# Optimization experiments

Measured on AMD Instinct MI355X. Metric: run time of the kernel, lower is better.

Reference implementation:

```python
import jax, jax.numpy as jnp
import numpy as np

K = 3
KK = K * K
PAD = 1          # kernel_size // 2
MAX_SHIFT = 8.0  # bias_range > 0
DEG = 2          # degrees = (2, 2), paon_type 'a'


def setup_inputs() -> dict:
    key = jax.random.key(0)
    ks = jax.random.split(key, 6)
    B, C, O, H, W = 4, 64, 64, 160, 160
    x = jax.random.normal(ks[0], (B, C, H, W), jnp.float32)
    # offset conv is 1x1: weight [2*K*K, C], bias [2*K*K]
    off_w = jax.random.normal(ks[1], (2 * KK, C), jnp.float32) * 0.1
    off_b = jax.random.normal(ks[2], (2 * KK,), jnp.float32) * 0.1
    scale = 1.0 / np.sqrt(C * KK).astype(np.float32)
    w_m = jax.random.normal(ks[3], (DEG * O, C, K, K), jnp.float32) * scale
    w_n = jax.random.normal(ks[4], (DEG * O, C, K, K), jnp.float32) * scale
    w0 = jax.random.normal(ks[5], (O,), jnp.float32) * 0.1
    return {"x": x, "off_w": off_w, "off_b": off_b, "w_m": w_m, "w_n": w_n, "w0": w0}


def _bilinear_sample(x, py, px):
    """x: [B,C,H,W]; py,px: [B,KK,H,W] -> [B,C,KK,H,W]; zero outside bounds."""
    B, C, H, W = x.shape
    xf = x.reshape(B, C, H * W)
    y0 = jnp.floor(py)
    x0 = jnp.floor(px)
    wy = py - y0
    wx = px - x0
    y0i = y0.astype(jnp.int32)
    x0i = x0.astype(jnp.int32)
    out = jnp.zeros((B, C) + py.shape[1:], x.dtype)
    corners = ((0, 0, (1 - wy) * (1 - wx)), (0, 1, (1 - wy) * wx),
               (1, 0, wy * (1 - wx)), (1, 1, wy * wx))
    for dy, dx, wgt in corners:
        yy = y0i + dy
        xx = x0i + dx
        valid = (yy >= 0) & (yy < H) & (xx >= 0) & (xx < W)
        idx = jnp.clip(yy, 0, H - 1) * W + jnp.clip(xx, 0, W - 1)
        g = jax.vmap(lambda f, i: f[:, i])(xf, idx.reshape(B, -1))  # [B,C,KK*H*W]
        out = out + g.reshape(B, C, *py.shape[1:]) * (wgt * valid)[:, None]
    return out


def _after_poly_a(y, ch, o, take_abs):
    # channel reorder + groupwise sum, per PaLaBase.after_poly_a
    order = np.array([(k * ch) % (ch * o) + k // o for k in range(ch * o)])
    y = y[:, order].reshape(y.shape[0], ch, o, *y.shape[2:])
    return jnp.abs(y).sum(2) if take_abs else y.sum(2)


def reference(x, off_w, off_b, w_m, w_n, w0):
    B, C, H, W = x.shape
    O = w0.shape[0]
    # --- DeformOffset: 1x1 conv -> clamp to image -> tanh soft-limit ---
    off_r = jnp.einsum('bchw,oc->bohw', x, off_w) + off_b[None, :, None, None]
    gy = jnp.arange(H, dtype=x.dtype)[None, None, :, None]
    gx = jnp.arange(W, dtype=x.dtype)[None, None, None, :]
    oy = jnp.clip(off_r[:, 0::2], -gy, H - gy)  # [B,KK,H,W] (dy per kernel pos)
    ox = jnp.clip(off_r[:, 1::2], -gx, W - gx)  # [B,KK,H,W] (dx per kernel pos)
    soft = lambda o: jnp.where(jnp.abs(o) >= MAX_SHIFT,
                               MAX_SHIFT * jnp.tanh(o / MAX_SHIFT), o)
    oy, ox = soft(oy), soft(ox)
    # --- deformable sampling grid (stride=1, dilation=1, zero padding) ---
    kidx = jnp.arange(KK)
    kh = (kidx // K).astype(x.dtype)[None, :, None, None]
    kw = (kidx % K).astype(x.dtype)[None, :, None, None]
    base_y = (jnp.arange(H, dtype=x.dtype) - PAD)[None, None, :, None]
    base_x = (jnp.arange(W, dtype=x.dtype) - PAD)[None, None, None, :]
    py = base_y + kh + oy
    px = base_x + kw + ox
    samp = _bilinear_sample(x, py, px)  # [B,C,KK,H,W]
    # --- Pade numerator / denominator convs on the sampled tensor ---
    pm_raw = jnp.einsum('bckhw,ock->bohw', samp, w_m.reshape(DEG * O, C, KK))
    qn_raw = jnp.einsum('bckhw,ock->bohw', samp, w_n.reshape(DEG * O, C, KK))
    pm = _after_poly_a(pm_raw, O, DEG, take_abs=False)
    qn = _after_poly_a(qn_raw, O, DEG, take_abs=True)
    # prepare_for_div_a: (pm + w0, 1 + qn)
    return (pm + w0[None, :, None, None]) / (1.0 + qn)
```

## Files before the change

kernel.cpp:

```cpp
#include <hip/hip_runtime.h>
#include <hip/hip_bf16.h>
#include <hip/hip_fp16.h>

#define Hh 160
#define Ww 160
#define Cc 64
#define HWc 25600
#define Bb 4
#define AST 76

typedef __attribute__((ext_vector_type(8))) _Float16 half8;
typedef __attribute__((ext_vector_type(4))) float f32x4;

__device__ __forceinline__ unsigned int f2h2u(float a, float b) {
  __half2 h = __floats2half2_rn(a, b);
  return *(unsigned int*)&h;
}

__global__ __launch_bounds__(256) void k_prep(
    const float* __restrict__ x, const float* __restrict__ wm,
    const float* __restrict__ wn, const float* __restrict__ ow,
    unsigned short* __restrict__ xT, unsigned short* __restrict__ bf) {
  if (blockIdx.x < 400) {
    __shared__ unsigned short s[64][260];
    int wg = blockIdx.x;
    int b = wg / 100;
    int pix0 = (wg % 100) * 256;
    int l = threadIdx.x & 63, wv = threadIdx.x >> 6;
    const float* xb = x + (size_t)b * Cc * HWc + pix0;
#pragma unroll
    for (int i = 0; i < 16; i++) {
      int c = i * 4 + wv;
      float4 v = *(const float4*)&xb[(size_t)c * HWc + l * 4];
      *(uint2*)&s[c][l * 4] = make_uint2(f2h2u(v.x, v.y), f2h2u(v.z, v.w));
    }
    __syncthreads();
    int p = threadIdx.x;
    unsigned int w[32];
#pragma unroll
    for (int j = 0; j < 32; j++) {
      unsigned int a = s[2 * j][p];
      unsigned int bb = s[2 * j + 1][p];
      w[j] = (a & 0xffffu) | (bb << 16);
    }
    unsigned short* dst = xT + ((size_t)(b * HWc + pix0 + p)) * 64;
#pragma unroll
    for (int j = 0; j < 8; j++)
      ((uint4*)dst)[j] = make_uint4(w[4 * j], w[4 * j + 1], w[4 * j + 2], w[4 * j + 3]);
  } else {
    int i = (blockIdx.x - 400) * 256 + threadIdx.x;
    if (i < 9 * 2 * 12 * 64 * 8) {
      int j2 = i & 7;
      int lane = (i >> 3) & 63;
      int ntck = i >> 9;
      int nt = ntck % 12;
      int ck = ntck / 12;
      int kk = ck >> 1;
      int chunk = ck & 1;
      int n = nt * 16 + (lane & 15);
      int c = chunk * 32 + (lane >> 4) * 8 + j2;
      float v;
      if (n < 64)
        v = wm[(n * 64 + c) * 9 + kk] + wm[((n + 64) * 64 + c) * 9 + kk];
      else
        v = wn[((n - 64) * 64 + c) * 9 + kk];
      __half hv = __float2half_rn(v);
      bf[i] = *(unsigned short*)&hv;
    } else if (i < 9 * 2 * 12 * 64 * 8 + 2 * 2 * 64 * 8) {
      int j = i - 9 * 2 * 12 * 64 * 8;
      int j2 = j & 7;
      int lane = (j >> 3) & 63;
      int rest = j >> 9;
      int ntile = rest & 1;
      int chunk = rest >> 1;
      int n = ntile * 16 + (lane & 15);
      int c = chunk * 32 + (lane >> 4) * 8 + j2;
      if (n < 18) {
        __half hv = __float2half_rn(ow[n * 64 + c]);
        bf[i] = *(unsigned short*)&hv;
      } else {
        bf[i] = 0;
      }
    }
  }
}

__device__ __forceinline__ void gather2h(const char* __restrict__ gbase, uint4 D,
                                         int chB, uint4& c00, uint4& c01,
                                         uint4& c10, uint4& c11, __half2& W00,
                                         __half2& W01, __half2& W10,
                                         __half2& W11) {
  int bb = (int)D.x + chB;
  int dxB = (int)(D.y & 0xffffu);
  int dyB = (int)(D.y >> 16);
  c00 = *(const uint4*)(gbase + bb);
  c01 = *(const uint4*)(gbase + bb + dxB);
  c10 = *(const uint4*)(gbase + bb + dyB);
  c11 = *(const uint4*)(gbase + bb + dxB + dyB);
  __half2 wz = *(const __half2*)&D.z;
  __half2 ww = *(const __half2*)&D.w;
  W00 = __half2half2(__low2half(wz));
  W01 = __half2half2(__high2half(wz));
  W10 = __half2half2(__low2half(ww));
  W11 = __half2half2(__high2half(ww));
}

__device__ __forceinline__ void combine_write(unsigned short* Arow,
                                              const uint4& c00, const uint4& c01,
                                              const uint4& c10, const uint4& c11,
                                              __half2 W00, __half2 W01,
                                              __half2 W10, __half2 W11) {
  const unsigned int* a = (const unsigned int*)&c00;
  const unsigned int* b = (const unsigned int*)&c01;
  const unsigned int* c = (const unsigned int*)&c10;
  const unsigned int* d = (const unsigned int*)&c11;
  unsigned int o[4];
#pragma unroll
  for (int j = 0; j < 4; j++) {
    __half2 ha = *(const __half2*)&a[j];
    __half2 hb = *(const __half2*)&b[j];
    __half2 hc = *(const __half2*)&c[j];
    __half2 hd = *(const __half2*)&d[j];
    __half2 r = __hfma2(ha, W00,
                        __hfma2(hb, W01, __hfma2(hc, W10, __hmul2(hd, W11))));
    o[j] = *(unsigned int*)&r;
  }
  *(uint4*)Arow = make_uint4(o[0], o[1], o[2], o[3]);
}

__global__ __launch_bounds__(256, 4) void k_main(
    const unsigned short* __restrict__ xT, const float* __restrict__ w0,
    const float* __restrict__ off_b, const unsigned short* __restrict__ bfrag,
    const unsigned short* __restrict__ obfrag, float* __restrict__ out) {
  __shared__ unsigned short A[2][64 * AST];
  __shared__ uint4 gdesc[576];
  float2* spy = (float2*)&A[0][0];
  const int tid = threadIdx.x;
  const int wg = blockIdx.x;
  const int band = wg & 7;
  const int local = wg >> 3;
  const int b = local / 50;
  const int pix0 = band * 3200 + (local % 50) * 64;
  const int wv = tid >> 6;
  const int l = tid & 63;
  const int lm = l & 15;
  const int quad = l >> 4;
  const int ch8 = l & 7;
  const int pr = l >> 3;
  const int chB = ch8 * 16;

  const unsigned short* xTb = xT + (size_t)b * HWc * 64;
  const char* gbase = (const char*)xTb;

  f32x4 acc[3][4];
  const f32x4 zero = {0.f, 0.f, 0.f, 0.f};
#pragma unroll
  for (int j = 0; j < 3; j++)
#pragma unroll
    for (int pt = 0; pt < 4; pt++) acc[j][pt] = zero;

  {
    f32x4 aO0 = zero, aO1 = zero;
    const unsigned short* xrow = xTb + (size_t)(pix0 + wv * 16 + lm) * 64;
#pragma unroll
    for (int chunk = 0; chunk < 2; chunk++) {
      half8 sb = *(const half8*)(xrow + chunk * 32 + quad * 8);
      half8 wf0 = *(const half8*)&obfrag[((chunk * 2 + 0) * 64 + l) * 8];
      half8 wf1 = *(const half8*)&obfrag[((chunk * 2 + 1) * 64 + l) * 8];
      aO0 = __builtin_amdgcn_mfma_f32_16x16x32_f16(wf0, sb, aO0, 0, 0, 0);
      aO1 = __builtin_amdgcn_mfma_f32_16x16x32_f16(wf1, sb, aO1, 0, 0, 0);
    }
    int pix = pix0 + wv * 16 + lm;
    int h = pix / Ww, w = pix % Ww;
    float fh = (float)h, fw = (float)w;
#pragma unroll
    for (int rr = 0; rr < 2; rr++) {
      int n = quad * 4 + 2 * rr;
      int kk = n >> 1;
      float oy = aO0[2 * rr] + off_b[n];
      float ox = aO0[2 * rr + 1] + off_b[n + 1];
      oy = fminf(fmaxf(oy, -fh), 160.0f - fh);
      ox = fminf(fmaxf(ox, -fw), 160.0f - fw);
      if (fabsf(oy) >= 8.0f) oy = 8.0f * tanhf(oy * 0.125f);
      if (fabsf(ox) >= 8.0f) ox = 8.0f * tanhf(ox * 0.125f);
      spy[kk * 64 + wv * 16 + lm] =
          make_float2(fh - 1.0f + (float)(kk / 3) + oy,
                      fw - 1.0f + (float)(kk % 3) + ox);
    }
    if (quad == 0) {
      float oy = aO1[0] + off_b[16];
      float ox = aO1[1] + off_b[17];
      oy = fminf(fmaxf(oy, -fh), 160.0f - fh);
      ox = fminf(fmaxf(ox, -fw), 160.0f - fw);
      if (fabsf(oy) >= 8.0f) oy = 8.0f * tanhf(oy * 0.125f);
      if (fabsf(ox) >= 8.0f) ox = 8.0f * tanhf(ox * 0.125f);
      spy[8 * 64 + wv * 16 + lm] =
          make_float2(fh + 1.0f + oy, fw + 1.0f + ox);
    }
  }
  __syncthreads();

  for (int e = tid; e < 576; e += 256) {
    float2 P = spy[e];
    float py = P.x, pxv = P.y;
    float y0f = floorf(py), x0f = floorf(pxv);
    float wy = py - y0f, wx = pxv - x0f;
    int y0 = (int)y0f, x0 = (int)x0f;
    float vy0 = (y0 >= 0 && y0 < Hh) ? 1.f : 0.f;
    float vy1 = (y0 >= -1 && y0 < Hh - 1) ? 1.f : 0.f;
    float vx0 = (x0 >= 0 && x0 < Ww) ? 1.f : 0.f;
    float vx1 = (x0 >= -1 && x0 < Ww - 1) ? 1.f : 0.f;
    int r0 = min(max(y0, 0), Hh - 1);
    int r1 = min(max(y0 + 1, 0), Hh - 1);
    int c0 = min(max(x0, 0), Ww - 1);
    int c1 = min(max(x0 + 1, 0), Ww - 1);
    float w00 = (1.f - wy) * (1.f - wx) * vy0 * vx0;
    float w01 = (1.f - wy) * wx * vy0 * vx1;
    float w10 = wy * (1.f - wx) * vy1 * vx0;
    float w11 = wy * wx * vy1 * vx1;
    uint4 D;
    D.x = (unsigned int)((r0 * Ww + c0) * 128);
    D.y = (unsigned int)((c1 - c0) * 128) |
          ((unsigned int)((r1 - r0) * Ww * 128) << 16);
    D.z = f2h2u(w00, w01);
    D.w = f2h2u(w10, w11);
    gdesc[e] = D;
  }
  __syncthreads();

#pragma unroll
  for (int i = 0; i < 2; i++) {
    int pl = wv * 16 + i * 8 + pr;
    uint4 c00, c01, c10, c11;
    __half2 W00, W01, W10, W11;
    gather2h(gbase, gdesc[pl], chB, c00, c01, c10, c11, W00, W01, W10, W11);
    combine_write(&A[0][pl * AST + ch8 * 8], c00, c01, c10, c11, W00, W01, W10,
                  W11);
  }
  __syncthreads();

  for (int kk = 0; kk < 9; kk++) {
    const int cur = kk & 1;
    uint4 g00[2], g01[2], g10[2], g11[2];
    __half2 W00[2], W01[2], W10[2], W11[2];
    if (kk < 8) {
#pragma unroll
      for (int i = 0; i < 2; i++) {
        int pl = wv * 16 + i * 8 + pr;
        gather2h(gbase, gdesc[(kk + 1) * 64 + pl], chB, g00[i], g01[i], g10[i],
                 g11[i], W00[i], W01[i], W10[i], W11[i]);
      }
    }
#pragma unroll
    for (int chunk = 0; chunk < 2; chunk++) {
      half8 sfr[4];
#pragma unroll
      for (int pt = 0; pt < 4; pt++)
        sfr[pt] = *(const half8*)&A[cur][(pt * 16 + lm) * AST + chunk * 32 +
                                         quad * 8];
      half8 wfr[3];
#pragma unroll
      for (int j = 0; j < 3; j++) {
        int nt = j * 4 + wv;
        wfr[j] = *(const half8*)&bfrag[((size_t)((kk * 2 + chunk) * 12 + nt) *
                                           64 + l) * 8];
      }
#pragma unroll
      for (int j = 0; j < 3; j++)
#pragma unroll
        for (int pt = 0; pt < 4; pt++)
          acc[j][pt] = __builtin_amdgcn_mfma_f32_16x16x32_f16(
              wfr[j], sfr[pt], acc[j][pt], 0, 0, 0);
    }
    if (kk < 8) {
#pragma unroll
      for (int i = 0; i < 2; i++) {
        int pl = wv * 16 + i * 8 + pr;
        combine_write(&A[cur ^ 1][pl * AST + ch8 * 8], g00[i], g01[i], g10[i],
                      g11[i], W00[i], W01[i], W10[i], W11[i]);
      }
    }
    __syncthreads();
  }

  float w0v[4];
#pragma unroll
  for (int r = 0; r < 4; r++) w0v[r] = w0[wv * 16 + quad * 4 + r];
  float* ob = out + (size_t)b * Cc * HWc + pix0;
#pragma unroll
  for (int pt = 0; pt < 4; pt++) {
#pragma unroll
    for (int r = 0; r < 4; r++) {
      int oc = wv * 16 + quad * 4 + r;
      float pm = acc[0][pt][r] + w0v[r];
      float qn = 1.0f + fabsf(acc[1][pt][r]) + fabsf(acc[2][pt][r]);
      ob[oc * HWc + pt * 16 + lm] = pm / qn;
    }
  }
}

extern "C" void kernel_launch(void* const* d_in, const int* in_sizes, int n_in,
                              void* d_out, int out_size, void* d_ws, size_t ws_size,
                              hipStream_t stream) {
  const float* x = (const float*)d_in[0];
  const float* off_w = (const float*)d_in[1];
  const float* off_b = (const float*)d_in[2];
  const float* w_m = (const float*)d_in[3];
  const float* w_n = (const float*)d_in[4];
  const float* w0 = (const float*)d_in[5];
  float* out = (float*)d_out;

  unsigned short* bfrag = (unsigned short*)d_ws;
  unsigned short* obfrag = (unsigned short*)((char*)d_ws + (size_t)221184);
  unsigned short* xT = (unsigned short*)((char*)d_ws + (size_t)225280);

  hipLaunchKernelGGL(k_prep, dim3(840), dim3(256), 0, stream, x, w_m, w_n,
                     off_w, xT, bfrag);
  hipLaunchKernelGGL(k_main, dim3(1600), dim3(256), 0, stream, xT, w0, off_b,
                     bfrag, obfrag, out);
}
```

Baseline: 126.6 us.

## Process two kernel taps per barrier with doubled LDS staging buffers

The sampled-tile LDS buffer gains a second slot per stage, so each pipeline step gathers and computes two kernel positions before one __syncthreads, cutting the barrier count from nine to five. The prefetch distance becomes two taps and the loop is fully unrolled. In exchange LDS use rises (about 19KB more per block), which may lower occupancy at the 4-blocks-per-CU launch bound, and register pressure increases from the unrolling.

After: 132.3 us. 1.05x slower.

```diff
diff --git a/kernel.cpp b/kernel.cpp
--- a/kernel.cpp
+++ b/kernel.cpp
@@ -132,9 +132,9 @@
     const unsigned short* __restrict__ xT, const float* __restrict__ w0,
     const float* __restrict__ off_b, const unsigned short* __restrict__ bfrag,
     const unsigned short* __restrict__ obfrag, float* __restrict__ out) {
-  __shared__ unsigned short A[2][64 * AST];
+  __shared__ unsigned short A[2][2][64 * AST];
   __shared__ uint4 gdesc[576];
-  float2* spy = (float2*)&A[0][0];
+  float2* spy = (float2*)&A[0][0][0];
   const int tid = threadIdx.x;
   const int wg = blockIdx.x;
   const int band = wg & 7;
@@ -229,55 +229,66 @@
   __syncthreads();
 
 #pragma unroll
-  for (int i = 0; i < 2; i++) {
-    int pl = wv * 16 + i * 8 + pr;
-    uint4 c00, c01, c10, c11;
-    __half2 W00, W01, W10, W11;
-    gather2h(gbase, gdesc[pl], chB, c00, c01, c10, c11, W00, W01, W10, W11);
-    combine_write(&A[0][pl * AST + ch8 * 8], c00, c01, c10, c11, W00, W01, W10,
-                  W11);
+  for (int sub = 0; sub < 2; sub++) {
+#pragma unroll
+    for (int i = 0; i < 2; i++) {
+      int pl = wv * 16 + i * 8 + pr;
+      uint4 c00, c01, c10, c11;
+      __half2 W00, W01, W10, W11;
+      gather2h(gbase, gdesc[sub * 64 + pl], chB, c00, c01, c10, c11, W00, W01,
+               W10, W11);
+      combine_write(&A[0][sub][pl * AST + ch8 * 8], c00, c01, c10, c11, W00,
+                    W01, W10, W11);
+    }
   }
   __syncthreads();
 
-  for (int kk = 0; kk < 9; kk++) {
-    const int cur = kk & 1;
-    uint4 g00[2], g01[2], g10[2], g11[2];
-    __half2 W00[2], W01[2], W10[2], W11[2];
-    if (kk < 8) {
-#pragma unroll
-      for (int i = 0; i < 2; i++) {
-        int pl = wv * 16 + i * 8 + pr;
-        gather2h(gbase, gdesc[(kk + 1) * 64 + pl], chB, g00[i], g01[i], g10[i],
-                 g11[i], W00[i], W01[i], W10[i], W11[i]);
+#pragma unroll
+  for (int r = 0; r < 5; r++) {
+    const int cur = r & 1;
+#pragma unroll
+    for (int sub = 0; sub < 2; sub++) {
+      const int kkv = 2 * r + sub;
+      const int nxt = kkv + 2;
+      if (kkv >= 9) continue;
+      uint4 g00[2], g01[2], g10[2], g11[2];
+      __half2 W00[2], W01[2], W10[2], W11[2];
+      if (nxt < 9) {
+#pragma unroll
+        for (int i = 0; i < 2; i++) {
+          int pl = wv * 16 + i * 8 + pr;
+          gather2h(gbase, gdesc[nxt * 64 + pl], chB, g00[i], g01[i], g10[i],
+                   g11[i], W00[i], W01[i], W10[i], W11[i]);
+        }
       }
-    }
-#pragma unroll
-    for (int chunk = 0; chunk < 2; chunk++) {
-      half8 sfr[4];
-#pragma unroll
-      for (int pt = 0; pt < 4; pt++)
-        sfr[pt] = *(const half8*)&A[cur][(pt * 16 + lm) * AST + chunk * 32 +
-                                         quad * 8];
-      half8 wfr[3];
-#pragma unroll
-      for (int j = 0; j < 3; j++) {
-        int nt = j * 4 + wv;
-        wfr[j] = *(const half8*)&bfrag[((size_t)((kk * 2 + chunk) * 12 + nt) *
-                                           64 + l) * 8];
+#pragma unroll
+      for (int chunk = 0; chunk < 2; chunk++) {
+        half8 sfr[4];
+#pragma unroll
+        for (int pt = 0; pt < 4; pt++)
+          sfr[pt] = *(const half8*)&A[cur][sub][(pt * 16 + lm) * AST +
+                                               chunk * 32 + quad * 8];
+        half8 wfr[3];
+#pragma unroll
+        for (int j = 0; j < 3; j++) {
+          int nt = j * 4 + wv;
+          wfr[j] = *(const half8*)&bfrag[((size_t)((kkv * 2 + chunk) * 12 + nt) *
+                                             64 + l) * 8];
+        }
+#pragma unroll
+        for (int j = 0; j < 3; j++)
+#pragma unroll
+          for (int pt = 0; pt < 4; pt++)
+            acc[j][pt] = __builtin_amdgcn_mfma_f32_16x16x32_f16(
+                wfr[j], sfr[pt], acc[j][pt], 0, 0, 0);
       }
-#pragma unroll
-      for (int j = 0; j < 3; j++)
-#pragma unroll
-        for (int pt = 0; pt < 4; pt++)
-          acc[j][pt] = __builtin_amdgcn_mfma_f32_16x16x32_f16(
-              wfr[j], sfr[pt], acc[j][pt], 0, 0, 0);
-    }
-    if (kk < 8) {
-#pragma unroll
-      for (int i = 0; i < 2; i++) {
-        int pl = wv * 16 + i * 8 + pr;
-        combine_write(&A[cur ^ 1][pl * AST + ch8 * 8], g00[i], g01[i], g10[i],
-                      g11[i], W00[i], W01[i], W10[i], W11[i]);
+      if (nxt < 9) {
+#pragma unroll
+        for (int i = 0; i < 2; i++) {
+          int pl = wv * 16 + i * 8 + pr;
+          combine_write(&A[cur ^ 1][sub][pl * AST + ch8 * 8], g00[i], g01[i],
+                        g10[i], g11[i], W00[i], W01[i], W10[i], W11[i]);
+        }
       }
     }
     __syncthreads();
```
